# Performance work log

Hardware: AMD Instinct MI355X
Metric: run time of the kernel (lower is better)

The kernel has to match this reference:

```python
import jax, jax.numpy as jnp
import numpy as np

DIM = 64  # per-head feature dim used for the 1/sqrt(dim) scale


def setup_inputs() -> dict:
    key = jax.random.key(0)
    kq, kk, kv, kw, kb = jax.random.split(key, 5)
    B, S, D, DK = 32, 4096, 64, 256
    q = jax.random.normal(kq, (B, S, D), dtype=jnp.float32)
    k = jax.random.normal(kk, (B, S, D), dtype=jnp.float32)
    v = jax.random.normal(kv, (B, S, D), dtype=jnp.float32)
    # Linear(input_size=S -> dim_k=DK): weight [DK, S], bias [DK]
    E_w = jax.random.normal(kw, (DK, S), dtype=jnp.float32) * (1.0 / np.sqrt(S))
    E_b = jax.random.normal(kb, (DK,), dtype=jnp.float32) * 0.01
    return {"q": q, "k": k, "v": v, "E_w": E_w, "E_b": E_b}


def reference(q, k, v, E_w, E_b):
    # K projection: k.transpose(1,2) -> [b, d, s]; E(k) -> [b, d, dim_k]
    K = jnp.einsum('bsd,ks->bdk', k, E_w) + E_b  # [b, d, dim_k]
    # scores = q @ K / sqrt(dim) -> [b, s, dim_k]
    scores = jnp.matmul(q, K) / jnp.sqrt(jnp.asarray(DIM, q.dtype))
    P_bar = jax.nn.softmax(scores, axis=-1)  # softmax over projected dim_k axis
    # V projection with F = E (parameter sharing): v -> [b, d, dim_k] -> transpose -> [b, dim_k, d]
    V = jnp.einsum('bsd,ks->bkd', v, E_w) + E_b[None, :, None]  # [b, dim_k, d]
    out = jnp.matmul(P_bar, V)  # [b, s, d]
    return out
```

## Files before the change

kernel.cpp:

```cpp
#include <hip/hip_runtime.h>
#include <hip/hip_bf16.h>
#include <stdint.h>

#define B_  32
#define S_  4096
#define D_  64
#define DK_ 256

typedef float f32x4 __attribute__((ext_vector_type(4)));
typedef short s16x8 __attribute__((ext_vector_type(8)));
typedef uint32_t u32x4 __attribute__((ext_vector_type(4)));

static __device__ __forceinline__ uint16_t f2bf(float f) {
    union { float f; uint32_t u; } x; x.f = f;
    uint32_t u = x.u;
    u += 0x7FFFu + ((u >> 16) & 1u);
    return (uint16_t)(u >> 16);
}

static __device__ __forceinline__ uint32_t pk2(float a, float b) {
    __hip_bfloat162 h = __float22bfloat162_rn(float2{a, b});
    union { __hip_bfloat162 h; uint32_t u; } c; c.h = h;
    return c.u;
}

static __device__ __forceinline__ void gload_lds16(const uint16_t* g, uint16_t* l) {
    __builtin_amdgcn_global_load_lds(
        (const __attribute__((address_space(1))) uint32_t*)g,
        (__attribute__((address_space(3))) uint32_t*)l, 16, 0, 0);
}

__global__ __launch_bounds__(256) void ewcvt(const float* __restrict__ E_w,
                                             uint16_t* __restrict__ Ewb) {
    const int idx = (blockIdx.x * 256 + threadIdx.x) * 8;
    const float4 f0 = *(const float4*)(E_w + idx);
    const float4 f1 = *(const float4*)(E_w + idx + 4);
    s16x8 o;
    o[0] = (short)f2bf(f0.x); o[1] = (short)f2bf(f0.y);
    o[2] = (short)f2bf(f0.z); o[3] = (short)f2bf(f0.w);
    o[4] = (short)f2bf(f1.x); o[5] = (short)f2bf(f1.y);
    o[6] = (short)f2bf(f1.z); o[7] = (short)f2bf(f1.w);
    *(s16x8*)(Ewb + idx) = o;
}

__global__ __launch_bounds__(256) void proj_mfma(
        const uint16_t* __restrict__ Ewb,
        const float* __restrict__ kin, const float* __restrict__ vin,
        float* __restrict__ part) {
    const int bid = blockIdx.x;
    const int ss = bid & 7;
    const int b  = (bid >> 3) & 31;
    const int p  = bid >> 8;
    const float* x = (p ? vin : kin) + (size_t)b * S_ * D_;
    float* outp = part + ((size_t)((p*32 + b)*8 + ss)) * (DK_ * D_);

    __shared__ __align__(16) uint16_t lds0[20 * 512];
    __shared__ __align__(16) uint16_t lds1[20 * 512];

    const int tid  = threadIdx.x;
    const int w    = tid >> 6;
    const int lane = tid & 63;
    const int l16  = lane & 15;
    const int grp  = lane >> 4;

    const int s0 = ss * 512 + grp * 8;
    const uint16_t* srcA[4];
    #pragma unroll
    for (int i = 0; i < 4; ++i)
        srcA[i] = Ewb + (size_t)((w*4 + i)*16 + l16) * S_ + s0;

    const int dcol = tid & 63;
    const float* srcB = x + ((size_t)(ss*512 + w*8)) * D_ + dcol;
    const int boff = 16*512 + (dcol >> 4)*512 + (w*16 + (dcol & 15))*8;

    f32x4 acc[4][4] = {};

    {
        float xv[8];
        #pragma unroll
        for (int i = 0; i < 8; ++i) xv[i] = srcB[i * D_];
        #pragma unroll
        for (int i = 0; i < 4; ++i)
            gload_lds16(srcA[i], &lds0[(w*4 + i) * 512]);
        s16x8 h;
        #pragma unroll
        for (int i = 0; i < 8; ++i) h[i] = (short)f2bf(xv[i]);
        *(s16x8*)&lds0[boff] = h;
    }
    __syncthreads();

    #pragma unroll
    for (int t = 0; t < 16; ++t) {
        uint16_t* cur = (t & 1) ? lds1 : lds0;
        uint16_t* nxt = (t & 1) ? lds0 : lds1;

        float xv[8];
        if (t + 1 < 16) {
            const float* sB = srcB + (size_t)(t+1)*32*D_;
            #pragma unroll
            for (int i = 0; i < 8; ++i) xv[i] = sB[i * D_];
            #pragma unroll
            for (int i = 0; i < 4; ++i)
                gload_lds16(srcA[i] + (t+1)*32, &nxt[(w*4 + i) * 512]);
        }

        s16x8 bf[4];
        #pragma unroll
        for (int nt = 0; nt < 4; ++nt)
            bf[nt] = *(const s16x8*)&cur[(16 + nt) * 512 + lane*8];
        #pragma unroll
        for (int m = 0; m < 4; ++m) {
            const s16x8 af = *(const s16x8*)&cur[(w*4 + m) * 512 + lane*8];
            #pragma unroll
            for (int nt = 0; nt < 4; ++nt)
                acc[m][nt] = __builtin_amdgcn_mfma_f32_16x16x32_bf16(af, bf[nt], acc[m][nt], 0, 0, 0);
        }

        if (t + 1 < 16) {
            s16x8 h;
            #pragma unroll
            for (int i = 0; i < 8; ++i) h[i] = (short)f2bf(xv[i]);
            *(s16x8*)&nxt[boff] = h;
        }
        __syncthreads();
    }

    #pragma unroll
    for (int m = 0; m < 4; ++m)
        #pragma unroll
        for (int nt = 0; nt < 4; ++nt)
            #pragma unroll
            for (int r = 0; r < 4; ++r)
                outp[(size_t)(w*64 + m*16 + grp*4 + r) * D_ + nt*16 + l16] =
                    acc[m][nt][r];
}

__global__ __launch_bounds__(256) void bias_reduce(
        const float* __restrict__ part, const float* __restrict__ E_b,
        uint16_t* __restrict__ Kbf, uint16_t* __restrict__ Vbf) {
    const int b   = blockIdx.x >> 2;
    const int kkt = blockIdx.x & 3;
    const int t   = threadIdx.x;

    __shared__ uint16_t Vt[64][66];

    const float* Kp = part + ((size_t)(b*8)) * 16384 + kkt*64*64;
    const float* Vp = part + ((size_t)((32 + b)*8)) * 16384 + kkt*64*64;

    #pragma unroll
    for (int j = 0; j < 8; ++j) {
        const int idx  = j*512 + t*2;
        const int kk_l = idx >> 6;
        const int d0   = idx & 63;
        float sk0 = 0.f, sk1 = 0.f, sv0 = 0.f, sv1 = 0.f;
        #pragma unroll
        for (int s = 0; s < 8; ++s) {
            const float2 k2 = *(const float2*)(Kp + s*16384 + kk_l*64 + d0);
            const float2 v2 = *(const float2*)(Vp + s*16384 + kk_l*64 + d0);
            sk0 += k2.x; sk1 += k2.y; sv0 += v2.x; sv1 += v2.y;
        }
        const float bias = E_b[kkt*64 + kk_l];
        const uint32_t kw = (uint32_t)f2bf(sk0 + bias) |
                            ((uint32_t)f2bf(sk1 + bias) << 16);
        *(uint32_t*)(Kbf + ((size_t)(b*256 + kkt*64 + kk_l))*64 + d0) = kw;
        Vt[kk_l][d0]     = f2bf(sv0 + bias);
        Vt[kk_l][d0 + 1] = f2bf(sv1 + bias);
    }
    __syncthreads();

    const int d = t & 63;
    const int c = t >> 6;
    uint16_t* vout = Vbf + (((size_t)(b*64 + d)) << 8) + kkt*64 + c*16;
    s16x8 o0, o1;
    #pragma unroll
    for (int i = 0; i < 8; ++i) {
        o0[i] = (short)Vt[c*16 + i][d];
        o1[i] = (short)Vt[c*16 + 8 + i][d];
    }
    *(s16x8*)vout       = o0;
    *(s16x8*)(vout + 8) = o1;
}

__global__ __launch_bounds__(512, 4) void attn(
        const float* __restrict__ q,
        const uint16_t* __restrict__ Kbf, const uint16_t* __restrict__ Vbf,
        float* __restrict__ out) {
    const int wg   = blockIdx.x;
    const int st   = wg & 31;
    const int b    = wg >> 5;
    const int tid  = threadIdx.x;
    const int wave = tid >> 6;
    const int lane = tid & 63;
    const int l16  = lane & 15;
    const int grp  = lane >> 4;
    const int s0   = st * 128 + wave * 16;

    __shared__ __align__(16) uint16_t Klds[16384];
    __shared__ __align__(16) uint16_t Vlds[16384];

    const uint16_t* Kb = Kbf + (size_t)b * DK_ * D_;
    const uint16_t* Vb = Vbf + (size_t)b * D_ * DK_;

    #pragma unroll
    for (int i = 0; i < 4; ++i) {
        const int s  = wave*4 + i;
        const int nt = s >> 1, kt = s & 1;
        gload_lds16(Kb + (size_t)(nt*16 + l16) * D_ + kt*32 + grp*8, &Klds[s*512]);
    }
    #pragma unroll
    for (int i = 0; i < 4; ++i) {
        const int s   = wave*4 + i;
        const int kt2 = s >> 2, nt2 = s & 3;
        gload_lds16(Vb + (size_t)(nt2*16 + l16) * DK_ + kt2*32 + grp*8, &Vlds[s*512]);
    }

    s16x8 qb[2];
    {
        const float* qp = q + ((size_t)b * S_ + s0 + l16) * D_;
        #pragma unroll
        for (int kt = 0; kt < 2; ++kt) {
            const int d0 = kt*32 + grp*8;
            const float4 f0 = *(const float4*)(qp + d0);
            const float4 f1 = *(const float4*)(qp + d0 + 4);
            s16x8 a;
            a[0] = (short)f2bf(f0.x * 0.125f);
            a[1] = (short)f2bf(f0.y * 0.125f);
            a[2] = (short)f2bf(f0.z * 0.125f);
            a[3] = (short)f2bf(f0.w * 0.125f);
            a[4] = (short)f2bf(f1.x * 0.125f);
            a[5] = (short)f2bf(f1.y * 0.125f);
            a[6] = (short)f2bf(f1.z * 0.125f);
            a[7] = (short)f2bf(f1.w * 0.125f);
            qb[kt] = a;
        }
    }

    __syncthreads();

    f32x4 acc[16] = {};
    #pragma unroll
    for (int nt = 0; nt < 16; ++nt) {
        #pragma unroll
        for (int kt = 0; kt < 2; ++kt) {
            const s16x8 kf = *(const s16x8*)&Klds[(nt*2 + kt)*512 + lane*8];
            acc[nt] = __builtin_amdgcn_mfma_f32_16x16x32_bf16(kf, qb[kt], acc[nt], 0, 0, 0);
        }
    }

    float sm = 0.f;
    #pragma unroll
    for (int nt = 0; nt < 16; ++nt) {
        #pragma unroll
        for (int r = 0; r < 4; ++r) {
            const float e = __expf(acc[nt][r]);
            acc[nt][r] = e;
            sm += e;
        }
    }
    sm += __shfl_xor(sm, 16);
    sm += __shfl_xor(sm, 32);
    const float inv = 1.f / sm;

    uint32_t pk[16][2];
    #pragma unroll
    for (int nt = 0; nt < 16; ++nt) {
        pk[nt][0] = pk2(acc[nt][0], acc[nt][1]);
        pk[nt][1] = pk2(acc[nt][2], acc[nt][3]);
    }

    float invs[4];
    #pragma unroll
    for (int r = 0; r < 4; ++r) invs[r] = __shfl(inv, grp*4 + r);

    const int sl0 = (((grp << 1) + 0) & 3) * 16 + l16;
    const int sl1 = (((grp << 1) + 1) & 3) * 16 + l16;
    const bool lohalf = (grp < 2);

    f32x4 o[4] = {};
    #pragma unroll
    for (int kt2 = 0; kt2 < 8; ++kt2) {
        union { u32x4 wv; s16x8 h; } u;
        #pragma unroll
        for (int c = 0; c < 4; ++c) {
            const int tt = c & 1;
            const int sl = (c >> 1) ? sl1 : sl0;
            const uint32_t lo = (uint32_t)__shfl((int)pk[2*kt2 + 0][tt], sl);
            const uint32_t hi = (uint32_t)__shfl((int)pk[2*kt2 + 1][tt], sl);
            u.wv[c] = lohalf ? lo : hi;
        }
        #pragma unroll
        for (int nt2 = 0; nt2 < 4; ++nt2) {
            const s16x8 vf = *(const s16x8*)&Vlds[(kt2*4 + nt2)*512 + lane*8];
            o[nt2] = __builtin_amdgcn_mfma_f32_16x16x32_bf16(u.h, vf, o[nt2], 0, 0, 0);
        }
    }

    #pragma unroll
    for (int nt2 = 0; nt2 < 4; ++nt2)
        #pragma unroll
        for (int r = 0; r < 4; ++r)
            out[((size_t)b * S_ + s0 + grp*4 + r) * D_ + nt2*16 + l16] =
                o[nt2][r] * invs[r];
}

extern "C" void kernel_launch(void* const* d_in, const int* in_sizes, int n_in,
                              void* d_out, int out_size, void* d_ws, size_t ws_size,
                              hipStream_t stream) {
    const float* q   = (const float*)d_in[0];
    const float* k   = (const float*)d_in[1];
    const float* v   = (const float*)d_in[2];
    const float* E_w = (const float*)d_in[3];
    const float* E_b = (const float*)d_in[4];
    float* out = (float*)d_out;

    char* ws = (char*)d_ws;
    float*    part = (float*)(ws);
    uint16_t* Kbf  = (uint16_t*)(ws + (32u << 20));
    uint16_t* Vbf  = (uint16_t*)(ws + (33u << 20));
    uint16_t* Ewb  = (uint16_t*)(ws + (34u << 20));

    ewcvt<<<512, 256, 0, stream>>>(E_w, Ewb);
    proj_mfma<<<512, 256, 0, stream>>>(Ewb, k, v, part);
    bias_reduce<<<128, 256, 0, stream>>>(part, E_b, Kbf, Vbf);
    attn<<<1024, 512, 0, stream>>>(q, Kbf, Vbf, out);
}
```

Baseline: 63.78 us.

## Split projection into 16 S-chunks and store bf16 transposed partials

The projection kernel now splits the sequence reduction into 16 chunks of 256 instead of 8 of 512, doubling the grid to 1024 blocks for better occupancy. Partial sums are stored as packed bf16 in a d-major layout, which halves partial-buffer traffic. The reduce kernel is reworked to sum 16 bf16 partials, write V directly, and transpose K through shared memory. Rounding partials to bf16 before summation adds accuracy loss, and the reduce kernel reads more partials.

Measured after the change: 72.09 us. +13.0%, slower.

```diff
diff --git a/kernel.cpp b/kernel.cpp
--- a/kernel.cpp
+++ b/kernel.cpp
@@ -16,6 +16,11 @@
     uint32_t u = x.u;
     u += 0x7FFFu + ((u >> 16) & 1u);
     return (uint16_t)(u >> 16);
+}
+
+static __device__ __forceinline__ float bf2f(uint32_t hi16) {
+    union { uint32_t u; float f; } x; x.u = hi16;
+    return x.f;
 }
 
 static __device__ __forceinline__ uint32_t pk2(float a, float b) {
@@ -46,13 +51,13 @@
 __global__ __launch_bounds__(256) void proj_mfma(
         const uint16_t* __restrict__ Ewb,
         const float* __restrict__ kin, const float* __restrict__ vin,
-        float* __restrict__ part) {
+        uint32_t* __restrict__ part) {
     const int bid = blockIdx.x;
-    const int ss = bid & 7;
-    const int b  = (bid >> 3) & 31;
-    const int p  = bid >> 8;
+    const int ss = bid & 15;
+    const int b  = (bid >> 4) & 31;
+    const int p  = bid >> 9;
     const float* x = (p ? vin : kin) + (size_t)b * S_ * D_;
-    float* outp = part + ((size_t)((p*32 + b)*8 + ss)) * (DK_ * D_);
+    uint32_t* outp = part + ((size_t)((p*32 + b)*16 + ss)) * 8192;
 
     __shared__ __align__(16) uint16_t lds0[20 * 512];
     __shared__ __align__(16) uint16_t lds1[20 * 512];
@@ -63,14 +68,14 @@
     const int l16  = lane & 15;
     const int grp  = lane >> 4;
 
-    const int s0 = ss * 512 + grp * 8;
+    const int s0 = ss * 256 + grp * 8;
     const uint16_t* srcA[4];
     #pragma unroll
     for (int i = 0; i < 4; ++i)
         srcA[i] = Ewb + (size_t)((w*4 + i)*16 + l16) * S_ + s0;
 
     const int dcol = tid & 63;
-    const float* srcB = x + ((size_t)(ss*512 + w*8)) * D_ + dcol;
+    const float* srcB = x + ((size_t)(ss*256 + w*8)) * D_ + dcol;
     const int boff = 16*512 + (dcol >> 4)*512 + (w*16 + (dcol & 15))*8;
 
     f32x4 acc[4][4] = {};
@@ -90,12 +95,12 @@
     __syncthreads();
 
     #pragma unroll
-    for (int t = 0; t < 16; ++t) {
+    for (int t = 0; t < 8; ++t) {
         uint16_t* cur = (t & 1) ? lds1 : lds0;
         uint16_t* nxt = (t & 1) ? lds0 : lds1;
 
         float xv[8];
-        if (t + 1 < 16) {
+        if (t + 1 < 8) {
             const float* sB = srcB + (size_t)(t+1)*32*D_;
             #pragma unroll
             for (int i = 0; i < 8; ++i) xv[i] = sB[i * D_];
@@ -116,7 +121,7 @@
                 acc[m][nt] = __builtin_amdgcn_mfma_f32_16x16x32_bf16(af, bf[nt], acc[m][nt], 0, 0, 0);
         }
 
-        if (t + 1 < 16) {
+        if (t + 1 < 8) {
             s16x8 h;
             #pragma unroll
             for (int i = 0; i < 8; ++i) h[i] = (short)f2bf(xv[i]);
@@ -126,59 +131,62 @@
     }
 
     #pragma unroll
-    for (int m = 0; m < 4; ++m)
-        #pragma unroll
-        for (int nt = 0; nt < 4; ++nt)
-            #pragma unroll
-            for (int r = 0; r < 4; ++r)
-                outp[(size_t)(w*64 + m*16 + grp*4 + r) * D_ + nt*16 + l16] =
-                    acc[m][nt][r];
+    for (int m = 0; m < 4; ++m) {
+        const int kkrow = w*64 + m*16 + grp*4;
+        #pragma unroll
+        for (int nt = 0; nt < 4; ++nt) {
+            const int didx = nt*16 + l16;
+            outp[didx*128 + (kkrow >> 1)]     = pk2(acc[m][nt][0], acc[m][nt][1]);
+            outp[didx*128 + (kkrow >> 1) + 1] = pk2(acc[m][nt][2], acc[m][nt][3]);
+        }
+    }
 }
 
 __global__ __launch_bounds__(256) void bias_reduce(
-        const float* __restrict__ part, const float* __restrict__ E_b,
+        const uint32_t* __restrict__ part, const float* __restrict__ E_b,
         uint16_t* __restrict__ Kbf, uint16_t* __restrict__ Vbf) {
-    const int b   = blockIdx.x >> 2;
-    const int kkt = blockIdx.x & 3;
-    const int t   = threadIdx.x;
-
-    __shared__ uint16_t Vt[64][66];
-
-    const float* Kp = part + ((size_t)(b*8)) * 16384 + kkt*64*64;
-    const float* Vp = part + ((size_t)((32 + b)*8)) * 16384 + kkt*64*64;
+    const int b  = blockIdx.x >> 2;
+    const int dt = blockIdx.x & 3;
+    const int t  = threadIdx.x;
+
+    __shared__ uint16_t Kt[256][18];
+
+    const uint32_t* Kp = part + ((size_t)(b*16))      * 8192 + dt*16*128;
+    const uint32_t* Vp = part + ((size_t)((32+b)*16)) * 8192 + dt*16*128;
 
     #pragma unroll
     for (int j = 0; j < 8; ++j) {
-        const int idx  = j*512 + t*2;
-        const int kk_l = idx >> 6;
-        const int d0   = idx & 63;
-        float sk0 = 0.f, sk1 = 0.f, sv0 = 0.f, sv1 = 0.f;
-        #pragma unroll
-        for (int s = 0; s < 8; ++s) {
-            const float2 k2 = *(const float2*)(Kp + s*16384 + kk_l*64 + d0);
-            const float2 v2 = *(const float2*)(Vp + s*16384 + kk_l*64 + d0);
-            sk0 += k2.x; sk1 += k2.y; sv0 += v2.x; sv1 += v2.y;
-        }
-        const float bias = E_b[kkt*64 + kk_l];
-        const uint32_t kw = (uint32_t)f2bf(sk0 + bias) |
-                            ((uint32_t)f2bf(sk1 + bias) << 16);
-        *(uint32_t*)(Kbf + ((size_t)(b*256 + kkt*64 + kk_l))*64 + d0) = kw;
-        Vt[kk_l][d0]     = f2bf(sv0 + bias);
-        Vt[kk_l][d0 + 1] = f2bf(sv1 + bias);
+        const int idx = j*256 + t;
+        const int d_l = idx >> 7;
+        const int kkp = idx & 127;
+        float k0 = 0.f, k1 = 0.f, v0 = 0.f, v1 = 0.f;
+        #pragma unroll
+        for (int s = 0; s < 16; ++s) {
+            const uint32_t ku = Kp[(size_t)s*8192 + d_l*128 + kkp];
+            const uint32_t vu = Vp[(size_t)s*8192 + d_l*128 + kkp];
+            k0 += bf2f(ku << 16);
+            k1 += bf2f(ku & 0xffff0000u);
+            v0 += bf2f(vu << 16);
+            v1 += bf2f(vu & 0xffff0000u);
+        }
+        const int kk0 = kkp*2;
+        const float b0 = E_b[kk0], b1 = E_b[kk0 + 1];
+        *(uint32_t*)(Vbf + ((size_t)(b*64 + dt*16 + d_l))*256 + kk0) =
+            (uint32_t)f2bf(v0 + b0) | ((uint32_t)f2bf(v1 + b1) << 16);
+        Kt[kk0][d_l]     = f2bf(k0 + b0);
+        Kt[kk0 + 1][d_l] = f2bf(k1 + b1);
     }
     __syncthreads();
 
-    const int d = t & 63;
-    const int c = t >> 6;
-    uint16_t* vout = Vbf + (((size_t)(b*64 + d)) << 8) + kkt*64 + c*16;
+    uint16_t* kout = Kbf + ((size_t)(b*256 + t))*64 + dt*16;
     s16x8 o0, o1;
     #pragma unroll
     for (int i = 0; i < 8; ++i) {
-        o0[i] = (short)Vt[c*16 + i][d];
-        o1[i] = (short)Vt[c*16 + 8 + i][d];
-    }
-    *(s16x8*)vout       = o0;
-    *(s16x8*)(vout + 8) = o1;
+        o0[i] = (short)Kt[t][i];
+        o1[i] = (short)Kt[t][8 + i];
+    }
+    *(s16x8*)kout       = o0;
+    *(s16x8*)(kout + 8) = o1;
 }
 
 __global__ __launch_bounds__(512, 4) void attn(
@@ -314,13 +322,13 @@
     float* out = (float*)d_out;
 
     char* ws = (char*)d_ws;
-    float*    part = (float*)(ws);
+    uint32_t* part = (uint32_t*)(ws);
     uint16_t* Kbf  = (uint16_t*)(ws + (32u << 20));
     uint16_t* Vbf  = (uint16_t*)(ws + (33u << 20));
     uint16_t* Ewb  = (uint16_t*)(ws + (34u << 20));
 
     ewcvt<<<512, 256, 0, stream>>>(E_w, Ewb);
-    proj_mfma<<<512, 256, 0, stream>>>(Ewb, k, v, part);
+    proj_mfma<<<1024, 256, 0, stream>>>(Ewb, k, v, part);
     bias_reduce<<<128, 256, 0, stream>>>(part, E_b, Kbf, Vbf);
     attn<<<1024, 512, 0, stream>>>(q, Kbf, Vbf, out);
 }
```
